# Performance work log

Measured on AMD Instinct MI355X. Metric: run time of the kernel, lower is better.

## Reference

```python
import jax, jax.numpy as jnp
import numpy as np


def setup_inputs() -> dict:
    key = jax.random.key(0)
    k1, k2, k3, k4 = jax.random.split(key, 4)
    B, S, IN, OUT = 4, 512, 4096, 11008
    x = jax.random.normal(k1, (B, S, IN), dtype=jnp.float32)
    # int8-valued weights stored as int32 (symmetric per-output-channel quant)
    w_int8 = jax.random.randint(k2, (OUT, IN), -128, 128, dtype=jnp.int32)
    # per-output-channel fp32 scales (positive, like absmax/127)
    scales = jax.random.uniform(k3, (OUT,), dtype=jnp.float32, minval=1e-4, maxval=0.05)
    bias = jax.random.normal(k4, (OUT,), dtype=jnp.float32)
    return {"x": x, "w_int8": w_int8, "scales": scales, "bias": bias}


def reference(x, w_int8, scales, bias):
    # On-the-fly dequant: w[o, i] = int8[o, i] * scale[o], then y = x @ w.T + b
    w = (w_int8.astype(jnp.float32) * scales[:, None]).astype(x.dtype)  # [OUT, IN]
    return jnp.einsum('bsi,oi->bso', x, w) + bias
```

## Files before the change

kernel.cpp:

```cpp
#include <hip/hip_runtime.h>
#include <hip/hip_bf16.h>
#include <stdint.h>


typedef __attribute__((ext_vector_type(8))) short short8;
typedef __attribute__((ext_vector_type(4))) float f32x4;
typedef __attribute__((ext_vector_type(4))) float float4v;
typedef __attribute__((ext_vector_type(4))) int int4v;

#define MM 2048
#define NN 11008
#define KK 4096
#define NT (KK / 64)
#define ROWB ((size_t)KK)

static __device__ __forceinline__ ushort f2bf_rne(float f) {
    uint32_t u = __builtin_bit_cast(uint32_t, f);
    u = (u + 0x7FFFu + ((u >> 16) & 1u)) >> 16;
    return (ushort)u;
}
static __device__ __forceinline__ ushort i2bf_exact(int v) {
    return (ushort)(__builtin_bit_cast(uint32_t, (float)v) >> 16);
}
static __device__ __forceinline__ void gload16(const void* g, void* lds) {
    __builtin_amdgcn_global_load_lds(
        (const __attribute__((address_space(1))) uint32_t*)g,
        (__attribute__((address_space(3))) uint32_t*)lds, 16, 0, 0);
}

__global__ __launch_bounds__(256)
void rowmax_x(const float* __restrict__ X, float* __restrict__ Sx, float* __restrict__ SxInv) {
    const int r = blockIdx.x;
    const float4v* xr = (const float4v*)(X + (size_t)r * KK);
    float m = 0.f;
    for (int i = threadIdx.x; i < KK / 4; i += 256) {
        float4v v = xr[i];
        m = fmaxf(m, fmaxf(fmaxf(fabsf(v[0]), fabsf(v[1])),
                           fmaxf(fabsf(v[2]), fabsf(v[3]))));
    }
#pragma unroll
    for (int off = 32; off; off >>= 1) m = fmaxf(m, __shfl_down(m, off));
    __shared__ float wmax[4];
    if ((threadIdx.x & 63) == 0) wmax[threadIdx.x >> 6] = m;
    __syncthreads();
    if (threadIdx.x == 0) {
        float a = fmaxf(fmaxf(wmax[0], wmax[1]), fmaxf(wmax[2], wmax[3]));
        Sx[r]    = a / 127.f;
        SxInv[r] = (a > 0.f) ? 127.f / a : 0.f;
    }
}

__global__ __launch_bounds__(256)
void quant_pack(const float* __restrict__ X, const int* __restrict__ W,
                const float* __restrict__ SxInv,
                char* __restrict__ Xq, char* __restrict__ Wq) {
    const int NX4 = MM * KK / 4;
    const int NW4 = NN * KK / 4;
    const int stride = gridDim.x * blockDim.x;
    for (int i = blockIdx.x * blockDim.x + threadIdx.x; i < NX4 + NW4; i += stride) {
        if (i < NX4) {
            float4v v = ((const float4v*)X)[i];
            const float inv = SxInv[i >> 10];
            uint32_t p = 0;
#pragma unroll
            for (int j = 0; j < 4; ++j) {
                int q = (int)rintf(v[j] * inv);
                p |= ((uint32_t)(q & 255)) << (8 * j);
            }
            ((uint32_t*)Xq)[i] = p;
        } else {
            int j = i - NX4;
            int4v w = ((const int4v*)W)[j];
            uint32_t p = ((uint32_t)(w[0] & 255)) | ((uint32_t)(w[1] & 255) << 8) |
                         ((uint32_t)(w[2] & 255) << 16) | ((uint32_t)(w[3] & 255) << 24);
            ((uint32_t*)Wq)[j] = p;
        }
    }
}

static __device__ __forceinline__ void stageA(const char* g, char* lds, int wid, size_t kb) {
    gload16(g + kb,                       lds + wid * 1024);
    gload16(g + kb + (size_t)128 * ROWB,  lds + 8192 + wid * 1024);
}
static __device__ __forceinline__ void stageB(const char* g, char* lds, int wid, size_t kb) {
    gload16(g + kb, lds + wid * 1024);
}

__global__ __launch_bounds__(512, 4)
void gemm_i8(const char* __restrict__ A, const char* __restrict__ B,
             const float* __restrict__ Sx, const float* __restrict__ S,
             const float* __restrict__ Bv, float* __restrict__ Y) {
    __shared__ char smem[49152];
    char* bA0 = smem;
    char* bA1 = smem + 16384;
    char* bB0 = smem + 32768;
    char* bB1 = smem + 40960;

    const int tid  = threadIdx.x;
    const int lane = tid & 63;
    const int wid  = tid >> 6;
    const int wm   = wid >> 1;
    const int wn   = wid & 1;
    const int l15  = lane & 15;
    const int q    = lane >> 4;

    const int swz  = (blockIdx.x & 7) * 86 + (blockIdx.x >> 3);
    const int brow = (swz / 86) * 256;
    const int bcol = (swz % 86) * 128;

    const int srow4 = tid >> 2;
    const int sslot = (tid & 3) ^ ((srow4 >> 1) & 3);
    const char* gA = A + (size_t)(brow + srow4) * ROWB + sslot * 16;
    const char* gB = B + (size_t)(bcol + srow4) * ROWB + sslot * 16;

    const int rdA = (wm * 64 + l15) * 64;
    const int rdB = (wn * 64 + l15) * 64;
    const int kq  = (q ^ ((l15 >> 1) & 3)) * 16;

#define LDA(buf, m) (*(const int4v*)((buf) + rdA + (m) * 1024 + kq))
#define LDB(buf, n) (*(const int4v*)((buf) + rdB + (n) * 1024 + kq))

    int4v acc[4][4] = {};

    stageA(gA, bA0, wid, 0);
    stageB(gB, bB0, wid, 0);
    stageA(gA, bA1, wid, 64);
    stageB(gB, bB1, wid, 64);
    asm volatile("s_waitcnt vmcnt(3)" ::: "memory");
    __builtin_amdgcn_s_barrier();

    char* curA = bA0; char* curB = bB0;
    char* nxtA = bA1; char* nxtB = bB1;

    for (int t = 0; t < NT; ++t) {
        const size_t kb2 = (size_t)((t + 2 < NT) ? t + 2 : NT - 1) * 64;

        int4v af[4], bf[4];
#pragma unroll
        for (int m = 0; m < 4; ++m) af[m] = LDA(curA, m);
#pragma unroll
        for (int n = 0; n < 4; ++n) bf[n] = LDB(curB, n);

        asm volatile("s_waitcnt lgkmcnt(0)" ::: "memory");
        __builtin_amdgcn_s_barrier();

        stageA(gA, curA, wid, kb2);
        stageB(gB, curB, wid, kb2);

        __builtin_amdgcn_s_setprio(1);
#pragma unroll
        for (int m = 0; m < 4; ++m)
#pragma unroll
            for (int n = 0; n < 4; ++n)
                acc[m][n] = __builtin_amdgcn_mfma_i32_16x16x64_i8(af[m], bf[n], acc[m][n], 0, 0, 0);
        __builtin_amdgcn_s_setprio(0);

        asm volatile("s_waitcnt vmcnt(3)" ::: "memory");
        __builtin_amdgcn_s_barrier();

        char* tA = curA; curA = nxtA; nxtA = tA;
        char* tB = curB; curB = nxtB; nxtB = tB;
    }

#pragma unroll
    for (int n = 0; n < 4; ++n) {
        const int gc = bcol + wn * 64 + n * 16 + l15;
        const float sj = S[gc];
        const float bj = Bv[gc];
#pragma unroll
        for (int m = 0; m < 4; ++m) {
            const int grow = brow + wm * 64 + m * 16 + q * 4;
            float* yp = Y + (size_t)grow * NN + gc;
#pragma unroll
            for (int r = 0; r < 4; ++r)
                yp[(size_t)r * NN] = (float)acc[m][n][r] * (Sx[grow + r] * sj) + bj;
        }
    }
#undef LDA
#undef LDB
}

#define BMF 128
#define BKF 32
#define LDW (BKF + 8)
__global__ __launch_bounds__(256, 2)
void int8lin_fused(const float* __restrict__ X, const int* __restrict__ W,
                   const float* __restrict__ S, const float* __restrict__ Bv,
                   float* __restrict__ Y) {
    __shared__ ushort As[BMF][LDW];
    __shared__ ushort Bs[BMF][LDW];
    const int tid = threadIdx.x, lane = tid & 63, wid = tid >> 6;
    const int wm = wid >> 1, wn = wid & 1, l15 = lane & 15, kh = (lane >> 4) * 8;
    const int bm = blockIdx.x & 15, bn = blockIdx.x >> 4;
    const int brow = bm * BMF, bcol = bn * BMF;
    const int srow = tid >> 1, scol = (tid & 1) * 16;
    const float* xg = X + (size_t)(brow + srow) * KK + scol;
    const int*   wg = W + (size_t)(bcol + srow) * KK + scol;
    f32x4 acc[4][4] = {};
    for (int kt = 0; kt < KK / BKF; ++kt) {
        float4v x0 = *(const float4v*)(xg + 0), x1 = *(const float4v*)(xg + 4);
        float4v x2 = *(const float4v*)(xg + 8), x3 = *(const float4v*)(xg + 12);
        int4v w0 = *(const int4v*)(wg + 0), w1 = *(const int4v*)(wg + 4);
        int4v w2 = *(const int4v*)(wg + 8), w3 = *(const int4v*)(wg + 12);
        xg += BKF; wg += BKF;
        short8 xa = { (short)f2bf_rne(x0[0]), (short)f2bf_rne(x0[1]), (short)f2bf_rne(x0[2]), (short)f2bf_rne(x0[3]),
                      (short)f2bf_rne(x1[0]), (short)f2bf_rne(x1[1]), (short)f2bf_rne(x1[2]), (short)f2bf_rne(x1[3]) };
        short8 xb = { (short)f2bf_rne(x2[0]), (short)f2bf_rne(x2[1]), (short)f2bf_rne(x2[2]), (short)f2bf_rne(x2[3]),
                      (short)f2bf_rne(x3[0]), (short)f2bf_rne(x3[1]), (short)f2bf_rne(x3[2]), (short)f2bf_rne(x3[3]) };
        short8 wa = { (short)i2bf_exact(w0[0]), (short)i2bf_exact(w0[1]), (short)i2bf_exact(w0[2]), (short)i2bf_exact(w0[3]),
                      (short)i2bf_exact(w1[0]), (short)i2bf_exact(w1[1]), (short)i2bf_exact(w1[2]), (short)i2bf_exact(w1[3]) };
        short8 wb = { (short)i2bf_exact(w2[0]), (short)i2bf_exact(w2[1]), (short)i2bf_exact(w2[2]), (short)i2bf_exact(w2[3]),
                      (short)i2bf_exact(w3[0]), (short)i2bf_exact(w3[1]), (short)i2bf_exact(w3[2]), (short)i2bf_exact(w3[3]) };
        __syncthreads();
        *(short8*)&As[srow][scol] = xa; *(short8*)&As[srow][scol + 8] = xb;
        *(short8*)&Bs[srow][scol] = wa; *(short8*)&Bs[srow][scol + 8] = wb;
        __syncthreads();
        short8 af[4], bf4[4];
#pragma unroll
        for (int i = 0; i < 4; ++i) af[i] = *(const short8*)&As[wm * 64 + i * 16 + l15][kh];
#pragma unroll
        for (int j = 0; j < 4; ++j) bf4[j] = *(const short8*)&Bs[wn * 64 + j * 16 + l15][kh];
#pragma unroll
        for (int i = 0; i < 4; ++i)
#pragma unroll
            for (int j = 0; j < 4; ++j)
                acc[i][j] = __builtin_amdgcn_mfma_f32_16x16x32_bf16(af[i], bf4[j], acc[i][j], 0, 0, 0);
    }
#pragma unroll
    for (int j = 0; j < 4; ++j) {
        const int gc = bcol + wn * 64 + j * 16 + l15;
        const float sj = S[gc], bj = Bv[gc];
#pragma unroll
        for (int i = 0; i < 4; ++i) {
            const int grow = brow + wm * 64 + i * 16 + (lane >> 4) * 4;
            float* yp = Y + (size_t)grow * NN + gc;
#pragma unroll
            for (int r = 0; r < 4; ++r)
                yp[(size_t)r * NN] = acc[i][j][r] * sj + bj;
        }
    }
}

extern "C" void kernel_launch(void* const* d_in, const int* in_sizes, int n_in,
                              void* d_out, int out_size, void* d_ws, size_t ws_size,
                              hipStream_t stream) {
    const float* x = (const float*)d_in[0];
    const int*   w = (const int*)d_in[1];
    const float* s = (const float*)d_in[2];
    const float* b = (const float*)d_in[3];
    float* y = (float*)d_out;

    const size_t wq_b = (size_t)NN * KK;
    const size_t xq_b = (size_t)MM * KK;
    const size_t need = wq_b + xq_b + 2 * MM * sizeof(float) + 256;
    if (ws_size >= need) {
        char*  Wq    = (char*)d_ws;
        char*  Xq    = Wq + wq_b;
        float* Sx    = (float*)(Xq + xq_b);
        float* SxInv = Sx + MM;
        hipLaunchKernelGGL(rowmax_x,   dim3(MM),   dim3(256), 0, stream, x, Sx, SxInv);
        hipLaunchKernelGGL(quant_pack, dim3(4096), dim3(256), 0, stream, x, w, SxInv, Xq, Wq);
        hipLaunchKernelGGL(gemm_i8, dim3((MM / 256) * (NN / 128)), dim3(512), 0, stream,
                           Xq, Wq, Sx, s, b, y);
    } else {
        hipLaunchKernelGGL(int8lin_fused, dim3((MM / BMF) * (NN / BMF)), dim3(256), 0, stream,
                           x, w, s, b, y);
    }
}
```

Before: 165.3 us.

## Triple-buffer LDS tiles in int8 GEMM to drop the mid-iteration barrier

Adds a third LDS buffer for both A and B tiles, so global-to-LDS prefetches for tile t+2 go into a buffer nobody is reading. This removes the per-iteration lgkmcnt wait and barrier that used to sit between the LDS fragment reads and the prefetch issue, leaving one barrier per k-step. The cost is shared memory per block growing from 48KB to 72KB, which can lower the number of resident blocks per CU. A variable rename in the bf16 fallback kernel is cosmetic.

```diff
diff --git a/kernel.cpp b/kernel.cpp
--- a/kernel.cpp
+++ b/kernel.cpp
@@ -27,6 +27,8 @@
         (const __attribute__((address_space(1))) uint32_t*)g,
         (__attribute__((address_space(3))) uint32_t*)lds, 16, 0, 0);
 }
+
+#define BAR() do { asm volatile("" ::: "memory"); __builtin_amdgcn_s_barrier(); asm volatile("" ::: "memory"); } while (0)
 
 __global__ __launch_bounds__(256)
 void rowmax_x(const float* __restrict__ X, float* __restrict__ Sx, float* __restrict__ SxInv) {
@@ -90,11 +92,13 @@
 void gemm_i8(const char* __restrict__ A, const char* __restrict__ B,
              const float* __restrict__ Sx, const float* __restrict__ S,
              const float* __restrict__ Bv, float* __restrict__ Y) {
-    __shared__ char smem[49152];
+    __shared__ char smem[73728];
     char* bA0 = smem;
     char* bA1 = smem + 16384;
-    char* bB0 = smem + 32768;
-    char* bB1 = smem + 40960;
+    char* bA2 = smem + 32768;
+    char* bB0 = smem + 49152;
+    char* bB1 = smem + 57344;
+    char* bB2 = smem + 65536;
 
     const int tid  = threadIdx.x;
     const int lane = tid & 63;
@@ -127,25 +131,22 @@
     stageA(gA, bA1, wid, 64);
     stageB(gB, bB1, wid, 64);
     asm volatile("s_waitcnt vmcnt(3)" ::: "memory");
-    __builtin_amdgcn_s_barrier();
-
-    char* curA = bA0; char* curB = bB0;
-    char* nxtA = bA1; char* nxtB = bB1;
+    BAR();
+
+    char* cA = bA0; char* nA = bA1; char* pA = bA2;
+    char* cB = bB0; char* nB = bB1; char* pB = bB2;
 
     for (int t = 0; t < NT; ++t) {
         const size_t kb2 = (size_t)((t + 2 < NT) ? t + 2 : NT - 1) * 64;
 
         int4v af[4], bf[4];
 #pragma unroll
-        for (int m = 0; m < 4; ++m) af[m] = LDA(curA, m);
-#pragma unroll
-        for (int n = 0; n < 4; ++n) bf[n] = LDB(curB, n);
-
-        asm volatile("s_waitcnt lgkmcnt(0)" ::: "memory");
-        __builtin_amdgcn_s_barrier();
-
-        stageA(gA, curA, wid, kb2);
-        stageB(gB, curB, wid, kb2);
+        for (int m = 0; m < 4; ++m) af[m] = LDA(cA, m);
+#pragma unroll
+        for (int n = 0; n < 4; ++n) bf[n] = LDB(cB, n);
+
+        stageA(gA, pA, wid, kb2);
+        stageB(gB, pB, wid, kb2);
 
         __builtin_amdgcn_s_setprio(1);
 #pragma unroll
@@ -156,10 +157,11 @@
         __builtin_amdgcn_s_setprio(0);
 
         asm volatile("s_waitcnt vmcnt(3)" ::: "memory");
-        __builtin_amdgcn_s_barrier();
-
-        char* tA = curA; curA = nxtA; nxtA = tA;
-        char* tB = curB; curB = nxtB; nxtB = tB;
+        BAR();
+
+        char* tmp;
+        tmp = cA; cA = nA; nA = pA; pA = tmp;
+        tmp = cB; cB = nB; nB = pB; pB = tmp;
     }
 
 #pragma unroll
@@ -215,16 +217,16 @@
         *(short8*)&As[srow][scol] = xa; *(short8*)&As[srow][scol + 8] = xb;
         *(short8*)&Bs[srow][scol] = wa; *(short8*)&Bs[srow][scol + 8] = wb;
         __syncthreads();
-        short8 af[4], bf4[4];
-#pragma unroll
-        for (int i = 0; i < 4; ++i) af[i] = *(const short8*)&As[wm * 64 + i * 16 + l15][kh];
+        short8 af2[4], bf4[4];
+#pragma unroll
+        for (int i = 0; i < 4; ++i) af2[i] = *(const short8*)&As[wm * 64 + i * 16 + l15][kh];
 #pragma unroll
         for (int j = 0; j < 4; ++j) bf4[j] = *(const short8*)&Bs[wn * 64 + j * 16 + l15][kh];
 #pragma unroll
         for (int i = 0; i < 4; ++i)
 #pragma unroll
             for (int j = 0; j < 4; ++j)
-                acc[i][j] = __builtin_amdgcn_mfma_f32_16x16x32_bf16(af[i], bf4[j], acc[i][j], 0, 0, 0);
+                acc[i][j] = __builtin_amdgcn_mfma_f32_16x16x32_bf16(af2[i], bf4[j], acc[i][j], 0, 0, 0);
     }
 #pragma unroll
     for (int j = 0; j < 4; ++j) {
```

Measured after the change: 162.1 us. About the same (-1.9%).
